# Kernel optimization log

Measured on AMD Instinct MI355X. Metric: run time of the kernel, lower is better.

The kernel has to match this reference:

```python
import jax, jax.numpy as jnp
import numpy as np

N, E, HID, H, L, R = 20000, 160000, 512, 8, 4, 128
DK = HID // H
SCALE = 1.0 / np.sqrt(DK)
EPS = 1e-5


def setup_inputs() -> dict:
    key = jax.random.key(0)
    ks = jax.random.split(key, 24)
    p = lambda i, shape: jax.random.normal(ks[i], shape, jnp.float32) * 0.02
    return {
        'x': jax.random.normal(ks[0], (N, HID), jnp.float32),
        'relations': jax.random.randint(ks[1], (E,), 0, R),
        'src': jax.random.randint(ks[2], (E,), 0, N),
        'dst': jax.random.randint(ks[3], (E,), 0, N),
        'rel_embed': p(4, (R, HID)),
        'Wq': p(5, (L, HID, HID)), 'bq': jnp.zeros((L, HID), jnp.float32),
        'Wk': p(6, (L, HID, HID)), 'bk': jnp.zeros((L, HID), jnp.float32),
        'Wv': p(7, (L, HID, HID)), 'bv': jnp.zeros((L, HID), jnp.float32),
        'Wo': p(8, (L, HID, HID)), 'bo': jnp.zeros((L, HID), jnp.float32),
        'W1': p(9, (L, HID, 4 * HID)), 'b1': jnp.zeros((L, 4 * HID), jnp.float32),
        'W2': p(10, (L, 4 * HID, HID)), 'b2': jnp.zeros((L, HID), jnp.float32),
        'ln1_g': jnp.ones((L, HID), jnp.float32), 'ln1_b': jnp.zeros((L, HID), jnp.float32),
        'ln2_g': jnp.ones((L, HID), jnp.float32), 'ln2_b': jnp.zeros((L, HID), jnp.float32),
    }


def _ln(x, g, b):
    m = x.mean(-1, keepdims=True)
    v = jnp.square(x - m).mean(-1, keepdims=True)
    return (x - m) * jax.lax.rsqrt(v + EPS) * g + b


def _layer(x, rh, src, dst, Wq, bq, Wk, bk, Wv, bv, Wo, bo, W1, b1, W2, b2, g1, bb1, g2, bb2):
    # rh: (E, H, DK) per-edge relation features
    q = (x @ Wq + bq).reshape(N, H, DK)
    k = (x @ Wk + bk).reshape(N, H, DK)
    v = (x @ Wv + bv).reshape(N, H, DK)
    # edge score: ((k_src + r) . q_dst) / sqrt(d_k)   -> (E, H)
    score = jnp.einsum('ehd,ehd->eh', k[src] + rh, q[dst]) * SCALE
    # segment softmax over incoming edges of each dst node
    smax = jax.ops.segment_max(score, dst, num_segments=N)
    smax = jnp.where(jnp.isfinite(smax), smax, 0.0)  # nodes with no in-edges
    ex = jnp.exp(score - smax[dst])                   # (E, H)
    z = jax.ops.segment_sum(ex, dst, num_segments=N)  # (N, H)
    wv = jax.ops.segment_sum(ex[:, :, None] * (v[src] + rh), dst, num_segments=N)  # (N, H, DK)
    o = wv / (z[:, :, None] + 1e-9)
    o = o.reshape(N, HID) @ Wo + bo
    h = _ln(x + o, g1, bb1)
    ff = jax.nn.relu(h @ W1 + b1) @ W2 + b2
    return _ln(h + ff, g2, bb2)


def reference(x, relations, src, dst, rel_embed, Wq, bq, Wk, bk, Wv, bv, Wo, bo, W1, b1, W2, b2, ln1_g, ln1_b, ln2_g, ln2_b):
    lg_x = rel_embed[relations]            # (E, HID), shared across layers
    rh = lg_x.reshape(E, H, DK)
    for i in range(L):
        x = _layer(x, rh, src, dst, Wq[i], bq[i], Wk[i], bk[i], Wv[i], bv[i],
                   Wo[i], bo[i], W1[i], b1[i], W2[i], b2[i],
                   ln1_g[i], ln1_b[i], ln2_g[i], ln2_b[i])
    return x
```

## Files before the change

kernel.cpp:

```cpp
#include <hip/hip_runtime.h>
#include <cstdint>
#include <cstddef>

#define N_NODES 20000
#define N_EDGES 160000
#define HIDDEN  512
#define NHEAD   8
#define HDK     64
#define NLAYER  4
#define FFDIM   2048
#define ATT_SCALE 0.125f

typedef float  f4  __attribute__((ext_vector_type(4)));
typedef short  s8v __attribute__((ext_vector_type(8)));
typedef __bf16 b8v __attribute__((ext_vector_type(8)));

template <typename V>
__device__ inline auto mfma_try(V a, V b, f4 c, int)
    -> decltype(__builtin_amdgcn_mfma_f32_16x16x32_bf16(a, b, c, 0, 0, 0)) {
  return __builtin_amdgcn_mfma_f32_16x16x32_bf16(a, b, c, 0, 0, 0);
}
template <typename V>
__device__ inline f4 mfma_try(V a, V b, f4 c, long) {
  return __builtin_amdgcn_mfma_f32_16x16x32_bf16(
      __builtin_bit_cast(b8v, a), __builtin_bit_cast(b8v, b), c, 0, 0, 0);
}
__device__ inline f4 mfma_bf16(s8v a, s8v b, f4 c) { return mfma_try(a, b, c, 0); }

__device__ __forceinline__ unsigned short f2bf(float f) {
  unsigned u = __builtin_bit_cast(unsigned, f);
  u += 0x7FFFu + ((u >> 16) & 1u);
  return (unsigned short)(u >> 16);
}
__device__ __forceinline__ float bf2f(unsigned short u) {
  return __builtin_bit_cast(float, (unsigned)u << 16);
}

#define GLOAD_LDS16(gp, lp)                                                   \
  __builtin_amdgcn_global_load_lds(                                           \
      (const __attribute__((address_space(1))) void*)(gp),                    \
      (__attribute__((address_space(3))) void*)(lp), 16, 0, 0)

__global__ void transpose_cast_kernel(const float* __restrict__ in,
                                      unsigned short* __restrict__ out,
                                      int K, int N) {
  __shared__ float t[32][33];
  int tx = threadIdx.x, ty = threadIdx.y;
  int n0 = blockIdx.x * 32, k0 = blockIdx.y * 32;
#pragma unroll
  for (int i = 0; i < 32; i += 8)
    t[ty + i][tx] = in[(size_t)(k0 + ty + i) * N + n0 + tx];
  __syncthreads();
#pragma unroll
  for (int i = 0; i < 32; i += 8)
    out[(size_t)(n0 + ty + i) * K + k0 + tx] = f2bf(t[tx][ty + i]);
}

__global__ void cast_kernel(const float* __restrict__ in, unsigned short* __restrict__ out, int n) {
  int i = blockIdx.x * blockDim.x + threadIdx.x;
  if (i < n) out[i] = f2bf(in[i]);
}

__global__ void bias_concat_kernel(const float* __restrict__ a, const float* __restrict__ b,
                                   const float* __restrict__ c, float* __restrict__ out) {
  int i = threadIdx.x + blockIdx.x * blockDim.x;
  if (i < 512) out[i] = a[i];
  else if (i < 1024) out[i] = b[i - 512];
  else if (i < 1536) out[i] = c[i - 1024];
}

#define BM 128
#define BN 128
#define BK 64

template <bool OBF16>
__global__ __launch_bounds__(256) void gemm_bf16(
    const unsigned short* __restrict__ A, const unsigned short* __restrict__ Bt,
    const float* __restrict__ bias, void* __restrict__ Cp,
    int M, int K, int N, int relu) {
  __shared__ __align__(16) unsigned short smem[16384];
  unsigned short* As = smem;
  unsigned short* Bs = smem + 8192;
  int tid = threadIdx.x;
  int wave = tid >> 6, lane = tid & 63;
  int quad = lane >> 4, l16 = lane & 15;
  int wm = (wave >> 1) * 64, wn = (wave & 1) * 64;

  int T = gridDim.x * gridDim.y;
  int i = blockIdx.y * gridDim.x + blockIdx.x;
  int C = T >> 3;
  int w = (i < (C << 3)) ? ((i & 7) * C + (i >> 3)) : i;
  int bx = w % gridDim.x, by = w / gridDim.x;
  int m0 = by * BM, n0 = bx * BN;

  f4 acc[4][4];
#pragma unroll
  for (int i2 = 0; i2 < 4; ++i2)
#pragma unroll
    for (int j = 0; j < 4; ++j) acc[i2][j] = (f4){0.f, 0.f, 0.f, 0.f};

  int rbase = wave * 8 + (lane >> 3);
  int q8 = (lane & 7) ^ ((lane >> 3) & 7);
  const unsigned short* aptr[4];
  const unsigned short* bptr[4];
#pragma unroll
  for (int j = 0; j < 4; ++j) {
    int r = j * 32 + rbase;
    int gm = m0 + r; if (gm >= M) gm = M - 1;
    aptr[j] = A + (size_t)gm * K + q8 * 8;
    bptr[j] = Bt + (size_t)(n0 + r) * K + q8 * 8;
  }

  int nk = K >> 6;
  for (int ks = 0; ks < nk; ++ks) {
#pragma unroll
    for (int j = 0; j < 4; ++j)
      GLOAD_LDS16(aptr[j], &As[j * 2048 + wave * 512]);
#pragma unroll
    for (int j = 0; j < 4; ++j)
      GLOAD_LDS16(bptr[j], &Bs[j * 2048 + wave * 512]);
#pragma unroll
    for (int j = 0; j < 4; ++j) { aptr[j] += BK; bptr[j] += BK; }
    __syncthreads();
#pragma unroll
    for (int s = 0; s < 2; ++s) {
      s8v af[4], bfr[4];
#pragma unroll
      for (int i2 = 0; i2 < 4; ++i2) {
        int ra = wm + i2 * 16 + l16;
        int rb = wn + i2 * 16 + l16;
        af[i2]  = *(const s8v*)(&As[ra * 64 + ((((s << 2) | quad) ^ (ra & 7)) * 8)]);
        bfr[i2] = *(const s8v*)(&Bs[rb * 64 + ((((s << 2) | quad) ^ (rb & 7)) * 8)]);
      }
#pragma unroll
      for (int mi = 0; mi < 4; ++mi)
#pragma unroll
        for (int ni = 0; ni < 4; ++ni)
          acc[mi][ni] = mfma_bf16(af[mi], bfr[ni], acc[mi][ni]);
    }
    __syncthreads();
  }

  if constexpr (OBF16) {
    unsigned short* Cs = smem + wave * 1088;
    float bvv[4];
#pragma unroll
    for (int ni = 0; ni < 4; ++ni) bvv[ni] = bias[n0 + wn + ni * 16 + l16];
    int row_l = lane >> 2, cg = lane & 3;
#pragma unroll
    for (int mi = 0; mi < 4; ++mi) {
#pragma unroll
      for (int ni = 0; ni < 4; ++ni) {
#pragma unroll
        for (int r = 0; r < 4; ++r) {
          float val = acc[mi][ni][r] + bvv[ni];
          if (relu) val = fmaxf(val, 0.f);
          Cs[(quad * 4 + r) * 68 + ni * 16 + l16] = f2bf(val);
        }
      }
      s8v v0 = *(const s8v*)(&Cs[row_l * 68 + cg * 16]);
      s8v v1 = *(const s8v*)(&Cs[row_l * 68 + cg * 16 + 8]);
      int grow = m0 + wm + mi * 16 + row_l;
      if (grow < M) {
        unsigned short* cp = (unsigned short*)Cp + (size_t)grow * N + n0 + wn + cg * 16;
        *(s8v*)cp = v0;
        *(s8v*)(cp + 8) = v1;
      }
    }
  } else {
#pragma unroll
    for (int ni = 0; ni < 4; ++ni) {
      int col = n0 + wn + ni * 16 + l16;
      float bv = bias[col];
#pragma unroll
      for (int mi = 0; mi < 4; ++mi) {
#pragma unroll
        for (int r = 0; r < 4; ++r) {
          int row = m0 + wm + mi * 16 + quad * 4 + r;
          if (row < M) {
            float val = acc[mi][ni][r] + bv;
            if (relu) val = fmaxf(val, 0.f);
            ((float*)Cp)[(size_t)row * N + col] = val;
          }
        }
      }
    }
  }
}

__global__ void hist_kernel(const int* __restrict__ dst, int* __restrict__ cnt, int E) {
  int e = blockIdx.x * blockDim.x + threadIdx.x;
  if (e < E) atomicAdd(&cnt[dst[e]], 1);
}

__global__ void scan_kernel(const int* __restrict__ cnt, int* __restrict__ offs, int n) {
  __shared__ int sh[1024];
  __shared__ int carry_sh;
  int tid = threadIdx.x;
  if (tid == 0) carry_sh = 0;
  __syncthreads();
  for (int base = 0; base < n; base += 1024) {
    int v = (base + tid < n) ? cnt[base + tid] : 0;
    sh[tid] = v;
    __syncthreads();
    for (int s = 1; s < 1024; s <<= 1) {
      int t = (tid >= s) ? sh[tid - s] : 0;
      __syncthreads();
      sh[tid] += t;
      __syncthreads();
    }
    int carry = carry_sh;
    if (base + tid < n) offs[base + tid] = carry + sh[tid] - v;
    __syncthreads();
    if (tid == 1023) carry_sh = carry + sh[1023];
    __syncthreads();
  }
  if (tid == 0) offs[n] = carry_sh;
}

__global__ void scatter_kernel(const int* __restrict__ dst, const int* __restrict__ src,
                               const int* __restrict__ relations, const int* __restrict__ offs,
                               int* __restrict__ cursor, int* __restrict__ esrc,
                               int* __restrict__ erel, int E) {
  int e = blockIdx.x * blockDim.x + threadIdx.x;
  if (e < E) {
    int d = dst[e];
    int pos = offs[d] + atomicAdd(&cursor[d], 1);
    esrc[pos] = src[e];
    erel[pos] = relations[e];
  }
}

__global__ void edge_attn_kernel(const unsigned short* __restrict__ q,
                                 const unsigned short* __restrict__ k,
                                 const unsigned short* __restrict__ v,
                                 const float* __restrict__ rel,
                                 const int* __restrict__ offs,
                                 const int* __restrict__ esrc,
                                 const int* __restrict__ erel,
                                 unsigned short* __restrict__ o, int Nn, int STR) {
  int wid = (blockIdx.x * blockDim.x + threadIdx.x) >> 6;
  int lane = threadIdx.x & 63;
  if (wid >= Nn) return;
  int base = (lane >> 3) * HDK + (lane & 7) * 8;

  s8v qv = *(const s8v*)(q + (size_t)wid * STR + base);
  float qf[8];
#pragma unroll
  for (int j = 0; j < 8; ++j) qf[j] = bf2f((unsigned short)qv[j]);

  int beg = offs[wid], end = offs[wid + 1];
  float m = -1e30f, z = 0.f;
  float acc[8];
#pragma unroll
  for (int j = 0; j < 8; ++j) acc[j] = 0.f;

  for (int i = beg; i < end; ++i) {
    int s = esrc[i], r = erel[i];
    s8v kv = *(const s8v*)(k + (size_t)s * STR + base);
    const float* rr = rel + (size_t)r * HIDDEN + base;
    float4 r0 = *(const float4*)rr;
    float4 r1 = *(const float4*)(rr + 4);
    float rf[8] = {r0.x, r0.y, r0.z, r0.w, r1.x, r1.y, r1.z, r1.w};
    float p = 0.f;
#pragma unroll
    for (int j = 0; j < 8; ++j) p += (bf2f((unsigned short)kv[j]) + rf[j]) * qf[j];
    p += __shfl_xor(p, 1, 64);
    p += __shfl_xor(p, 2, 64);
    p += __shfl_xor(p, 4, 64);
    p *= ATT_SCALE;
    float mn = fmaxf(m, p);
    float a = __expf(m - mn);
    float w = __expf(p - mn);
    s8v vv = *(const s8v*)(v + (size_t)s * STR + base);
    z = z * a + w;
#pragma unroll
    for (int j = 0; j < 8; ++j)
      acc[j] = acc[j] * a + w * (bf2f((unsigned short)vv[j]) + rf[j]);
    m = mn;
  }
  float rz = 1.f / (z + 1e-9f);
  s8v ov;
#pragma unroll
  for (int j = 0; j < 8; ++j) ov[j] = (short)f2bf(acc[j] * rz);
  *(s8v*)(o + (size_t)wid * HIDDEN + base) = ov;
}

template <bool XF32, bool WF32>
__global__ void ln_kernel(const void* __restrict__ xp, const float* __restrict__ y,
                          const float* __restrict__ g, const float* __restrict__ b,
                          float* __restrict__ outf, unsigned short* __restrict__ outb, int Nn) {
  int wid = (blockIdx.x * blockDim.x + threadIdx.x) >> 6;
  int lane = threadIdx.x & 63;
  if (wid >= Nn) return;
  const float* yr = y + (size_t)wid * HIDDEN;
  float vals[8];
  float sum = 0.f;
#pragma unroll
  for (int j = 0; j < 8; ++j) {
    int idx = j * 64 + lane;
    float xv;
    if constexpr (XF32) xv = ((const float*)xp)[(size_t)wid * HIDDEN + idx];
    else                xv = bf2f(((const unsigned short*)xp)[(size_t)wid * HIDDEN + idx]);
    vals[j] = xv + yr[idx];
    sum += vals[j];
  }
#pragma unroll
  for (int off = 32; off; off >>= 1) sum += __shfl_xor(sum, off, 64);
  float mean = sum * (1.f / 512.f);
  float sq = 0.f;
#pragma unroll
  for (int j = 0; j < 8; ++j) { float d = vals[j] - mean; sq += d * d; }
#pragma unroll
  for (int off = 32; off; off >>= 1) sq += __shfl_xor(sq, off, 64);
  float rstd = rsqrtf(sq * (1.f / 512.f) + 1e-5f);
#pragma unroll
  for (int j = 0; j < 8; ++j) {
    int idx = j * 64 + lane;
    float val = (vals[j] - mean) * rstd * g[idx] + b[idx];
    if constexpr (WF32) outf[(size_t)wid * HIDDEN + idx] = val;
    outb[(size_t)wid * HIDDEN + idx] = f2bf(val);
  }
}

extern "C" void kernel_launch(void* const* d_in, const int* in_sizes, int n_in,
                              void* d_out, int out_size, void* d_ws, size_t ws_size,
                              hipStream_t stream) {
  const float* x0        = (const float*)d_in[0];
  const int*   relations = (const int*)d_in[1];
  const int*   src       = (const int*)d_in[2];
  const int*   dst       = (const int*)d_in[3];
  const float* rel_embed = (const float*)d_in[4];
  const float* Wq = (const float*)d_in[5];  const float* bq = (const float*)d_in[6];
  const float* Wk = (const float*)d_in[7];  const float* bk = (const float*)d_in[8];
  const float* Wv = (const float*)d_in[9];  const float* bv = (const float*)d_in[10];
  const float* Wo = (const float*)d_in[11]; const float* bo = (const float*)d_in[12];
  const float* W1 = (const float*)d_in[13]; const float* b1 = (const float*)d_in[14];
  const float* W2 = (const float*)d_in[15]; const float* b2 = (const float*)d_in[16];
  const float* g1  = (const float*)d_in[17]; const float* bb1 = (const float*)d_in[18];
  const float* g2  = (const float*)d_in[19]; const float* bb2 = (const float*)d_in[20];
  float* xout = (float*)d_out;

  const size_t S1 = 512 * 512;
  const size_t S2 = 512 * 2048;
  const size_t NH = (size_t)N_NODES * HIDDEN;

  unsigned short* wqkv = (unsigned short*)d_ws;
  unsigned short* wo = wqkv + 3 * S1;
  unsigned short* w1 = wo + S1;
  unsigned short* w2 = w1 + S2;
  float* bqkv = (float*)(w2 + S2);
  unsigned short* arena = (unsigned short*)(bqkv + 1536);
  unsigned short* qkvb = arena;
  unsigned short* ob   = arena + 3 * NH;
  unsigned short* ff1  = arena;
  float* proj = (float*)arena;
  unsigned short* hbb = arena + 4 * NH;
  unsigned short* xb  = hbb + NH;
  float* projf = (float*)(xb + NH);
  int* cnt    = (int*)(projf + NH);
  int* offs   = cnt + N_NODES;
  int* cursor = offs + N_NODES + 1;
  int* esrc   = cursor + N_NODES;
  int* erel   = esrc + N_EDGES;

  hipMemsetAsync(cnt, 0, N_NODES * sizeof(int), stream);
  hipMemsetAsync(cursor, 0, N_NODES * sizeof(int), stream);
  hist_kernel<<<(N_EDGES + 255) / 256, 256, 0, stream>>>(dst, cnt, N_EDGES);
  scan_kernel<<<1, 1024, 0, stream>>>(cnt, offs, N_NODES);
  scatter_kernel<<<(N_EDGES + 255) / 256, 256, 0, stream>>>(dst, src, relations, offs, cursor, esrc, erel, N_EDGES);

  cast_kernel<<<(int)((NH + 255) / 256), 256, 0, stream>>>(x0, xb, (int)NH);

  const int MBc = (N_NODES + BM - 1) / BM;
  dim3 tb(32, 8);

  for (int l = 0; l < NLAYER; ++l) {
    const float* x_in = (l == 0) ? x0 : xout;
    transpose_cast_kernel<<<dim3(16, 16), tb, 0, stream>>>(Wq + l * S1, wqkv, 512, 512);
    transpose_cast_kernel<<<dim3(16, 16), tb, 0, stream>>>(Wk + l * S1, wqkv + S1, 512, 512);
    transpose_cast_kernel<<<dim3(16, 16), tb, 0, stream>>>(Wv + l * S1, wqkv + 2 * S1, 512, 512);
    transpose_cast_kernel<<<dim3(16, 16), tb, 0, stream>>>(Wo + l * S1, wo, 512, 512);
    transpose_cast_kernel<<<dim3(64, 16), tb, 0, stream>>>(W1 + l * S2, w1, 512, 2048);
    transpose_cast_kernel<<<dim3(16, 64), tb, 0, stream>>>(W2 + l * S2, w2, 2048, 512);
    bias_concat_kernel<<<6, 256, 0, stream>>>(bq + l * 512, bk + l * 512, bv + l * 512, bqkv);
    gemm_bf16<true><<<dim3(12, MBc), 256, 0, stream>>>(xb, wqkv, bqkv, qkvb, N_NODES, 512, 1536, 0);
    edge_attn_kernel<<<(N_NODES + 3) / 4, 256, 0, stream>>>(qkvb, qkvb + 512, qkvb + 1024,
                                                            rel_embed, offs, esrc, erel, ob, N_NODES, 1536);
    gemm_bf16<false><<<dim3(4, MBc), 256, 0, stream>>>(ob, wo, bo + l * 512, proj, N_NODES, 512, 512, 0);
    ln_kernel<true, false><<<N_NODES / 4, 256, 0, stream>>>(x_in, proj, g1 + l * 512, bb1 + l * 512, nullptr, hbb, N_NODES);
    gemm_bf16<true><<<dim3(16, MBc), 256, 0, stream>>>(hbb, w1, b1 + l * 2048, ff1, N_NODES, 512, 2048, 1);
    gemm_bf16<false><<<dim3(4, MBc), 256, 0, stream>>>(ff1, w2, b2 + l * 512, projf, N_NODES, 2048, 512, 0);
    ln_kernel<false, true><<<N_NODES / 4, 256, 0, stream>>>(hbb, projf, g2 + l * 512, bb2 + l * 512, xout, xb, N_NODES);
  }
}
```

Baseline: 1.415 ms.

## Merge weight prep, use bf16 intermediates, and prefetch edges in attention

Seven per-layer weight transpose/bias kernels are folded into one launch. The Wo and W2 GEMM outputs and the relation embeddings are stored as bf16 instead of fp32, and LayerNorm reads the residual from the bf16 copy. The fp32 output is written only in the final layer. The edge attention loop software-prefetches the next edge's k, v and relation rows. Together these cut launch count and memory traffic, at the cost of some extra bf16 rounding in the residual path.

New measurement: 1.238 ms. 1.14x faster.

```diff
diff --git a/kernel.cpp b/kernel.cpp
--- a/kernel.cpp
+++ b/kernel.cpp
@@ -10,6 +10,8 @@
 #define NLAYER  4
 #define FFDIM   2048
 #define ATT_SCALE 0.125f
+#define S1C 262144
+#define S2C 1048576
 
 typedef float  f4  __attribute__((ext_vector_type(4)));
 typedef short  s8v __attribute__((ext_vector_type(8)));
@@ -41,32 +43,50 @@
       (const __attribute__((address_space(1))) void*)(gp),                    \
       (__attribute__((address_space(3))) void*)(lp), 16, 0, 0)
 
-__global__ void transpose_cast_kernel(const float* __restrict__ in,
-                                      unsigned short* __restrict__ out,
-                                      int K, int N) {
-  __shared__ float t[32][33];
-  int tx = threadIdx.x, ty = threadIdx.y;
-  int n0 = blockIdx.x * 32, k0 = blockIdx.y * 32;
-#pragma unroll
-  for (int i = 0; i < 32; i += 8)
-    t[ty + i][tx] = in[(size_t)(k0 + ty + i) * N + n0 + tx];
-  __syncthreads();
-#pragma unroll
-  for (int i = 0; i < 32; i += 8)
-    out[(size_t)(n0 + ty + i) * K + k0 + tx] = f2bf(t[tx][ty + i]);
-}
-
 __global__ void cast_kernel(const float* __restrict__ in, unsigned short* __restrict__ out, int n) {
   int i = blockIdx.x * blockDim.x + threadIdx.x;
   if (i < n) out[i] = f2bf(in[i]);
 }
 
-__global__ void bias_concat_kernel(const float* __restrict__ a, const float* __restrict__ b,
-                                   const float* __restrict__ c, float* __restrict__ out) {
-  int i = threadIdx.x + blockIdx.x * blockDim.x;
-  if (i < 512) out[i] = a[i];
-  else if (i < 1024) out[i] = b[i - 512];
-  else if (i < 1536) out[i] = c[i - 1024];
+__global__ void weight_prep_kernel(const float* __restrict__ Wq, const float* __restrict__ Wk,
+                                   const float* __restrict__ Wv, const float* __restrict__ Wo_,
+                                   const float* __restrict__ W1, const float* __restrict__ W2,
+                                   const float* __restrict__ bq, const float* __restrict__ bk,
+                                   const float* __restrict__ bv,
+                                   unsigned short* __restrict__ wqkv, unsigned short* __restrict__ wo,
+                                   unsigned short* __restrict__ w1, unsigned short* __restrict__ w2,
+                                   float* __restrict__ bqkv) {
+  int id = blockIdx.x;
+  if (id >= 3072) {
+    int i = (id - 3072) * 256 + threadIdx.y * 32 + threadIdx.x;
+    if (i < 512) bqkv[i] = bq[i];
+    else if (i < 1024) bqkv[i] = bk[i - 512];
+    else if (i < 1536) bqkv[i] = bv[i - 1024];
+    return;
+  }
+  const float* in; unsigned short* out; int K, N, bx, by;
+  if (id < 1024) {
+    int m = id >> 8, t = id & 255;
+    in = (m == 0) ? Wq : (m == 1) ? Wk : (m == 2) ? Wv : Wo_;
+    out = (m == 3) ? wo : wqkv + m * S1C;
+    K = 512; N = 512; bx = t & 15; by = t >> 4;
+  } else if (id < 2048) {
+    int t = id - 1024;
+    in = W1; out = w1; K = 512; N = 2048; bx = t & 63; by = t >> 6;
+  } else {
+    int t = id - 2048;
+    in = W2; out = w2; K = 2048; N = 512; bx = t & 15; by = t >> 4;
+  }
+  __shared__ float t32[32][33];
+  int tx = threadIdx.x, ty = threadIdx.y;
+  int n0 = bx * 32, k0 = by * 32;
+#pragma unroll
+  for (int i = 0; i < 32; i += 8)
+    t32[ty + i][tx] = in[(size_t)(k0 + ty + i) * N + n0 + tx];
+  __syncthreads();
+#pragma unroll
+  for (int i = 0; i < 32; i += 8)
+    out[(size_t)(n0 + ty + i) * K + k0 + tx] = f2bf(t32[tx][ty + i]);
 }
 
 #define BM 128
@@ -234,7 +254,7 @@
 __global__ void edge_attn_kernel(const unsigned short* __restrict__ q,
                                  const unsigned short* __restrict__ k,
                                  const unsigned short* __restrict__ v,
-                                 const float* __restrict__ rel,
+                                 const unsigned short* __restrict__ relb,
                                  const int* __restrict__ offs,
                                  const int* __restrict__ esrc,
                                  const int* __restrict__ erel,
@@ -255,28 +275,38 @@
 #pragma unroll
   for (int j = 0; j < 8; ++j) acc[j] = 0.f;
 
+  s8v kv = {}, vv = {}, rv = {};
+  if (beg < end) {
+    int s0 = esrc[beg], r0 = erel[beg];
+    kv = *(const s8v*)(k + (size_t)s0 * STR + base);
+    vv = *(const s8v*)(v + (size_t)s0 * STR + base);
+    rv = *(const s8v*)(relb + (size_t)r0 * HIDDEN + base);
+  }
   for (int i = beg; i < end; ++i) {
-    int s = esrc[i], r = erel[i];
-    s8v kv = *(const s8v*)(k + (size_t)s * STR + base);
-    const float* rr = rel + (size_t)r * HIDDEN + base;
-    float4 r0 = *(const float4*)rr;
-    float4 r1 = *(const float4*)(rr + 4);
-    float rf[8] = {r0.x, r0.y, r0.z, r0.w, r1.x, r1.y, r1.z, r1.w};
-    float p = 0.f;
-#pragma unroll
-    for (int j = 0; j < 8; ++j) p += (bf2f((unsigned short)kv[j]) + rf[j]) * qf[j];
+    s8v kc = kv, vc = vv, rc = rv;
+    if (i + 1 < end) {
+      int sn = esrc[i + 1], rn = erel[i + 1];
+      kv = *(const s8v*)(k + (size_t)sn * STR + base);
+      vv = *(const s8v*)(v + (size_t)sn * STR + base);
+      rv = *(const s8v*)(relb + (size_t)rn * HIDDEN + base);
+    }
+    float rf[8], p = 0.f;
+#pragma unroll
+    for (int j = 0; j < 8; ++j) {
+      rf[j] = bf2f((unsigned short)rc[j]);
+      p += (bf2f((unsigned short)kc[j]) + rf[j]) * qf[j];
+    }
     p += __shfl_xor(p, 1, 64);
     p += __shfl_xor(p, 2, 64);
     p += __shfl_xor(p, 4, 64);
     p *= ATT_SCALE;
     float mn = fmaxf(m, p);
     float a = __expf(m - mn);
-    float w = __expf(p - mn);
-    s8v vv = *(const s8v*)(v + (size_t)s * STR + base);
-    z = z * a + w;
+    float wgt = __expf(p - mn);
+    z = z * a + wgt;
 #pragma unroll
     for (int j = 0; j < 8; ++j)
-      acc[j] = acc[j] * a + w * (bf2f((unsigned short)vv[j]) + rf[j]);
+      acc[j] = acc[j] * a + wgt * (bf2f((unsigned short)vc[j]) + rf[j]);
     m = mn;
   }
   float rz = 1.f / (z + 1e-9f);
@@ -286,23 +316,19 @@
   *(s8v*)(o + (size_t)wid * HIDDEN + base) = ov;
 }
 
-template <bool XF32, bool WF32>
-__global__ void ln_kernel(const void* __restrict__ xp, const float* __restrict__ y,
+template <bool WF32>
+__global__ void ln_kernel(const unsigned short* __restrict__ xp, const unsigned short* __restrict__ y,
                           const float* __restrict__ g, const float* __restrict__ b,
                           float* __restrict__ outf, unsigned short* __restrict__ outb, int Nn) {
   int wid = (blockIdx.x * blockDim.x + threadIdx.x) >> 6;
   int lane = threadIdx.x & 63;
   if (wid >= Nn) return;
-  const float* yr = y + (size_t)wid * HIDDEN;
   float vals[8];
   float sum = 0.f;
 #pragma unroll
   for (int j = 0; j < 8; ++j) {
     int idx = j * 64 + lane;
-    float xv;
-    if constexpr (XF32) xv = ((const float*)xp)[(size_t)wid * HIDDEN + idx];
-    else                xv = bf2f(((const unsigned short*)xp)[(size_t)wid * HIDDEN + idx]);
-    vals[j] = xv + yr[idx];
+    vals[j] = bf2f(xp[(size_t)wid * HIDDEN + idx]) + bf2f(y[(size_t)wid * HIDDEN + idx]);
     sum += vals[j];
   }
 #pragma unroll
@@ -341,8 +367,8 @@
   const float* g2  = (const float*)d_in[19]; const float* bb2 = (const float*)d_in[20];
   float* xout = (float*)d_out;
 
-  const size_t S1 = 512 * 512;
-  const size_t S2 = 512 * 2048;
+  const size_t S1 = S1C;
+  const size_t S2 = S2C;
   const size_t NH = (size_t)N_NODES * HIDDEN;
 
   unsigned short* wqkv = (unsigned short*)d_ws;
@@ -354,11 +380,12 @@
   unsigned short* qkvb = arena;
   unsigned short* ob   = arena + 3 * NH;
   unsigned short* ff1  = arena;
-  float* proj = (float*)arena;
+  unsigned short* proj = arena;
   unsigned short* hbb = arena + 4 * NH;
   unsigned short* xb  = hbb + NH;
-  float* projf = (float*)(xb + NH);
-  int* cnt    = (int*)(projf + NH);
+  unsigned short* projb = xb + NH;
+  unsigned short* relb  = projb + NH;
+  int* cnt    = (int*)(relb + 65536);
   int* offs   = cnt + N_NODES;
   int* cursor = offs + N_NODES + 1;
   int* esrc   = cursor + N_NODES;
@@ -369,28 +396,27 @@
   hist_kernel<<<(N_EDGES + 255) / 256, 256, 0, stream>>>(dst, cnt, N_EDGES);
   scan_kernel<<<1, 1024, 0, stream>>>(cnt, offs, N_NODES);
   scatter_kernel<<<(N_EDGES + 255) / 256, 256, 0, stream>>>(dst, src, relations, offs, cursor, esrc, erel, N_EDGES);
-
   cast_kernel<<<(int)((NH + 255) / 256), 256, 0, stream>>>(x0, xb, (int)NH);
+  cast_kernel<<<256, 256, 0, stream>>>(rel_embed, relb, 65536);
 
   const int MBc = (N_NODES + BM - 1) / BM;
   dim3 tb(32, 8);
 
   for (int l = 0; l < NLAYER; ++l) {
-    const float* x_in = (l == 0) ? x0 : xout;
-    transpose_cast_kernel<<<dim3(16, 16), tb, 0, stream>>>(Wq + l * S1, wqkv, 512, 512);
-    transpose_cast_kernel<<<dim3(16, 16), tb, 0, stream>>>(Wk + l * S1, wqkv + S1, 512, 512);
-    transpose_cast_kernel<<<dim3(16, 16), tb, 0, stream>>>(Wv + l * S1, wqkv + 2 * S1, 512, 512);
-    transpose_cast_kernel<<<dim3(16, 16), tb, 0, stream>>>(Wo + l * S1, wo, 512, 512);
-    transpose_cast_kernel<<<dim3(64, 16), tb, 0, stream>>>(W1 + l * S2, w1, 512, 2048);
-    transpose_cast_kernel<<<dim3(16, 64), tb, 0, stream>>>(W2 + l * S2, w2, 2048, 512);
-    bias_concat_kernel<<<6, 256, 0, stream>>>(bq + l * 512, bk + l * 512, bv + l * 512, bqkv);
+    weight_prep_kernel<<<3078, tb, 0, stream>>>(Wq + l * S1, Wk + l * S1, Wv + l * S1, Wo + l * S1,
+                                                W1 + l * S2, W2 + l * S2,
+                                                bq + l * 512, bk + l * 512, bv + l * 512,
+                                                wqkv, wo, w1, w2, bqkv);
     gemm_bf16<true><<<dim3(12, MBc), 256, 0, stream>>>(xb, wqkv, bqkv, qkvb, N_NODES, 512, 1536, 0);
     edge_attn_kernel<<<(N_NODES + 3) / 4, 256, 0, stream>>>(qkvb, qkvb + 512, qkvb + 1024,
-                                                            rel_embed, offs, esrc, erel, ob, N_NODES, 1536);
-    gemm_bf16<false><<<dim3(4, MBc), 256, 0, stream>>>(ob, wo, bo + l * 512, proj, N_NODES, 512, 512, 0);
-    ln_kernel<true, false><<<N_NODES / 4, 256, 0, stream>>>(x_in, proj, g1 + l * 512, bb1 + l * 512, nullptr, hbb, N_NODES);
+                                                            relb, offs, esrc, erel, ob, N_NODES, 1536);
+    gemm_bf16<true><<<dim3(4, MBc), 256, 0, stream>>>(ob, wo, bo + l * 512, proj, N_NODES, 512, 512, 0);
+    ln_kernel<false><<<N_NODES / 4, 256, 0, stream>>>(xb, proj, g1 + l * 512, bb1 + l * 512, nullptr, hbb, N_NODES);
     gemm_bf16<true><<<dim3(16, MBc), 256, 0, stream>>>(hbb, w1, b1 + l * 2048, ff1, N_NODES, 512, 2048, 1);
-    gemm_bf16<false><<<dim3(4, MBc), 256, 0, stream>>>(ff1, w2, b2 + l * 512, projf, N_NODES, 2048, 512, 0);
-    ln_kernel<false, true><<<N_NODES / 4, 256, 0, stream>>>(hbb, projf, g2 + l * 512, bb2 + l * 512, xout, xb, N_NODES);
-  }
-}
+    gemm_bf16<true><<<dim3(4, MBc), 256, 0, stream>>>(ff1, w2, b2 + l * 512, projb, N_NODES, 2048, 512, 0);
+    if (l == NLAYER - 1)
+      ln_kernel<true><<<N_NODES / 4, 256, 0, stream>>>(hbb, projb, g2 + l * 512, bb2 + l * 512, xout, xb, N_NODES);
+    else
+      ln_kernel<false><<<N_NODES / 4, 256, 0, stream>>>(hbb, projb, g2 + l * 512, bb2 + l * 512, nullptr, xb, N_NODES);
+  }
+}
```
